# Kernel tuning notes

Measured on AMD Instinct MI355X. Metric: run time of the kernel, lower is better.

The kernel has to match this reference:

```python
import jax, jax.numpy as jnp
import numpy as np

BATCH = 32
N_LEVELS = (16384, 4096, 1024, 256)   # nodes at each mesh resolution
M_LEVELS = (4096, 1024, 256, 64)      # nodes after each Pool (downsample)
DEG = 6                               # directed edges per node
POOL_K = 3                            # nnz per row of downsample matrix
FILTERS = (3, 32, 32, 32, 64)         # channel chain of the 4 ChebConvs
K_CHEB = 6                            # Chebyshev polynomial order


def setup_inputs() -> dict:
    key = jax.random.key(0)
    ks = iter(jax.random.split(key, 64))
    inp = {"x": jax.random.normal(next(ks), (BATCH, N_LEVELS[0], FILTERS[0]), jnp.float32)}
    for i, N in enumerate(N_LEVELS):
        er = jnp.repeat(jnp.arange(N), DEG)
        off = jax.random.randint(next(ks), (N * DEG,), 1, N)
        inp[f"er{i}"] = er
        inp[f"ec{i}"] = (er + off) % N  # guaranteed no self loops
    for i, (M, N) in enumerate(zip(M_LEVELS, N_LEVELS)):
        inp[f"pr{i}"] = jnp.repeat(jnp.arange(M), POOL_K)
        inp[f"pc{i}"] = jax.random.randint(next(ks), (M * POOL_K,), 0, N)
        inp[f"pv{i}"] = jax.random.uniform(next(ks), (M * POOL_K,), jnp.float32)
    for i in range(4):
        fin, fout = FILTERS[i], FILTERS[i + 1]
        scale = 1.0 / np.sqrt(fin * K_CHEB)
        inp[f"W{i}"] = jax.random.normal(next(ks), (K_CHEB, fin, fout), jnp.float32) * scale
        inp[f"b{i}"] = jnp.zeros((fout,), jnp.float32)
    inp["enc_W"] = jax.random.normal(next(ks), (M_LEVELS[-1] * FILTERS[-1], 128), jnp.float32) * 0.1
    inp["enc_b"] = jnp.zeros((128,), jnp.float32)
    inp["cls_W"] = jax.random.normal(next(ks), (128, 10), jnp.float32) * 0.1
    inp["cls_b"] = jnp.zeros((10,), jnp.float32)
    return inp


def _cheb_conv(x, er, ec, W, b):
    # x: [B,N,Fin]; W: [K,Fin,Fout].
    # PyG ChebConv with lambda_max=2: L_hat = L - I = -D^{-1/2} A D^{-1/2}.
    N = x.shape[1]
    deg = jnp.zeros((N,), x.dtype).at[er].add(1.0)
    dinv = jnp.where(deg > 0, 1.0 / jnp.sqrt(jnp.maximum(deg, 1.0)), 0.0)
    norm = -(dinv[er] * dinv[ec])  # [E]

    def L(t):  # sparse matvec: gather neighbor feats, weight, scatter-add
        return jnp.zeros_like(t).at[:, er].add(t[:, ec] * norm[None, :, None])

    Tx0 = x
    out = jnp.einsum("bnf,fg->bng", Tx0, W[0])
    Tx1 = L(x)
    out = out + jnp.einsum("bnf,fg->bng", Tx1, W[1])
    for k in range(2, W.shape[0]):
        Tx2 = 2.0 * L(Tx1) - Tx0
        out = out + jnp.einsum("bnf,fg->bng", Tx2, W[k])
        Tx0, Tx1 = Tx1, Tx2
    return out + b


def _pool(x, pr, pc, pv, m):
    # sparse downsample matrix [m,N]: index_select cols * value, scatter_add rows
    B, _, F = x.shape
    return jnp.zeros((B, m, F), x.dtype).at[:, pr].add(x[:, pc] * pv[None, :, None])


def reference(x, er0, ec0, er1, ec1, er2, ec2, er3, ec3,
              pr0, pc0, pv0, pr1, pc1, pv1, pr2, pc2, pv2, pr3, pc3, pv3,
              W0, b0, W1, b1, W2, b2, W3, b3, enc_W, enc_b, cls_W, cls_b):
    ers, ecs = (er0, er1, er2, er3), (ec0, ec1, ec2, ec3)
    prs, pcs, pvs = (pr0, pr1, pr2, pr3), (pc0, pc1, pc2, pc3), (pv0, pv1, pv2, pv3)
    Ws, bs = (W0, W1, W2, W3), (b0, b1, b2, b3)
    for i in range(4):  # fixed n_layers loop (structurally distinct layers)
        x = jax.nn.relu(_cheb_conv(x, ers[i], ecs[i], Ws[i], bs[i]))
        x = _pool(x, prs[i], pcs[i], pvs[i], M_LEVELS[i])
    x = x.reshape(x.shape[0], -1)  # [B, 64*64]
    h = jax.nn.relu(x @ enc_W + enc_b)
    return h @ cls_W + cls_b
```

## Files before the change

kernel.cpp:

```cpp
#include <hip/hip_runtime.h>
#include <cstddef>
#include <cstdint>

#define BATCH 32


__device__ __forceinline__ void fma4(float4& a, float s, const float4& w) {
  a.x += s * w.x; a.y += s * w.y; a.z += s * w.z; a.w += s * w.w;
}
__device__ __forceinline__ float4 relu4(const float4& a) {
  return make_float4(fmaxf(a.x, 0.f), fmaxf(a.y, 0.f), fmaxf(a.z, 0.f), fmaxf(a.w, 0.f));
}

__global__ void __launch_bounds__(256) transpose_x(
    const float* __restrict__ x, float* __restrict__ xt)
{
  int t = blockIdx.x * 256 + threadIdx.x;
  int n = t / 96;
  int r = t % 96;
  int b = r / 3;
  int f = r - b * 3;
  xt[t] = x[((size_t)b * 16384 + n) * 3 + f];
}

template<int N, int R4>
__global__ void __launch_bounds__(256) cheb_step_nm(
    const float4* __restrict__ Tin, const float4* __restrict__ Tpp,
    const int* __restrict__ ec, float4* __restrict__ Tout,
    float coef, float beta)
{
  int idx = blockIdx.x * 256 + threadIdx.x;
  int n = idx / R4;
  int r = idx % R4;
  const int* e = ec + n * 6;
  float4 s = make_float4(0.f, 0.f, 0.f, 0.f);
#pragma unroll
  for (int d = 0; d < 6; ++d) {
    float4 v = Tin[(size_t)e[d] * R4 + r];
    s.x += v.x; s.y += v.y; s.z += v.z; s.w += v.w;
  }
  float4 p = Tpp[idx];
  float4 o;
  o.x = coef * s.x + beta * p.x;
  o.y = coef * s.y + beta * p.y;
  o.z = coef * s.z + beta * p.z;
  o.w = coef * s.w + beta * p.w;
  Tout[idx] = o;
}

template<int N, int F, int THREADS, int MINW>
__global__ void __launch_bounds__(THREADS, MINW) cheb_recur_reg(
    const float* __restrict__ X,
    const int* __restrict__ ec,
    float* __restrict__ T)
{
  constexpr int FS = 2;
  constexpr int NPT = N / THREADS;
  __shared__ float cur[N * FS];
  const float cI = -1.0f / 6.0f;
  const float cS = -1.0f / 3.0f;
  const int b = blockIdx.x & 31;
  const int fbase = (blockIdx.x >> 5) * FS;
  constexpr size_t SL = (size_t)N * 32 * F;
  float prevv[NPT][FS];
#pragma unroll
  for (int i = 0; i < NPT; ++i) {
    int n = threadIdx.x + i * THREADS;
    float2 v = *(const float2*)(X + ((size_t)n * 32 + b) * F + fbase);
    cur[n * FS + 0] = v.x;
    cur[n * FS + 1] = v.y;
  }
  __syncthreads();
#pragma unroll 1
  for (int k = 1; k <= 5; ++k) {
    float newv[NPT][FS];
    float* Tk = T + (size_t)(k - 1) * SL;
#pragma unroll
    for (int i = 0; i < NPT; ++i) {
      int n = threadIdx.x + i * THREADS;
      const int* e = ec + n * 6;
      float s0 = 0.f, s1 = 0.f;
#pragma unroll
      for (int d = 0; d < 6; ++d) {
        int c = e[d];
        s0 += cur[c * FS + 0];
        s1 += cur[c * FS + 1];
      }
      float v0, v1;
      if (k == 1) { v0 = cI * s0; v1 = cI * s1; }
      else        { v0 = cS * s0 - prevv[i][0]; v1 = cS * s1 - prevv[i][1]; }
      newv[i][0] = v0; newv[i][1] = v1;
      *(float2*)(Tk + ((size_t)n * 32 + b) * F + fbase) = make_float2(v0, v1);
    }
    __syncthreads();
#pragma unroll
    for (int i = 0; i < NPT; ++i) {
      int n = threadIdx.x + i * THREADS;
      prevv[i][0] = cur[n * FS + 0];
      prevv[i][1] = cur[n * FS + 1];
      cur[n * FS + 0] = newv[i][0];
      cur[n * FS + 1] = newv[i][1];
    }
    __syncthreads();
  }
}

template<int N, int M, int FOUT, bool OUT_BM>
__global__ void __launch_bounds__(256) pool_conv_f3(
    const float* __restrict__ X, const float* __restrict__ T,
    const float* __restrict__ W, const float* __restrict__ bias,
    const int* __restrict__ pc, const float* __restrict__ pv,
    float* __restrict__ out)
{
  constexpr int F4 = FOUT / 4;
  constexpr size_t SL = (size_t)N * BATCH * 3;
  __shared__ float Ws[6 * 3 * FOUT];
  for (int i = threadIdx.x; i < 6 * 3 * FOUT; i += 256) Ws[i] = W[i];
  __syncthreads();
  const float4* Ws4 = (const float4*)Ws;
  int t = blockIdx.x * 256 + threadIdx.x;
  int fo4 = t % F4;
  int b   = (t / F4) % BATCH;
  int m   = t / (F4 * BATCH);
  int c0 = pc[m * 3 + 0], c1 = pc[m * 3 + 1], c2 = pc[m * 3 + 2];
  float v0 = pv[m * 3 + 0], v1 = pv[m * 3 + 1], v2 = pv[m * 3 + 2];
  float4 bi = ((const float4*)bias)[fo4];
  float4 a0 = bi, a1 = bi, a2 = bi;
#pragma unroll
  for (int k = 0; k < 6; ++k) {
    const float* base = (k == 0) ? X : (T + (size_t)(k - 1) * SL);
    const float* r0 = base + ((size_t)c0 * BATCH + b) * 3;
    const float* r1 = base + ((size_t)c1 * BATCH + b) * 3;
    const float* r2 = base + ((size_t)c2 * BATCH + b) * 3;
#pragma unroll
    for (int f = 0; f < 3; ++f) {
      float4 w = Ws4[(k * 3 + f) * F4 + fo4];
      fma4(a0, r0[f], w);
      fma4(a1, r1[f], w);
      fma4(a2, r2[f], w);
    }
  }
  a0 = relu4(a0); a1 = relu4(a1); a2 = relu4(a2);
  float4 acc;
  acc.x = v0*a0.x + v1*a1.x + v2*a2.x;
  acc.y = v0*a0.y + v1*a1.y + v2*a2.y;
  acc.z = v0*a0.z + v1*a1.z + v2*a2.z;
  acc.w = v0*a0.w + v1*a1.w + v2*a2.w;
  size_t oi = OUT_BM ? (((size_t)b * M + m) * F4 + fo4) : (((size_t)m * BATCH + b) * F4 + fo4);
  ((float4*)out)[oi] = acc;
}

template<int N, int M, int FOUT, bool OUT_BM>
__global__ void __launch_bounds__(256) pool_conv_v32(
    const float* __restrict__ X, const float* __restrict__ T,
    const float* __restrict__ W, const float* __restrict__ bias,
    const int* __restrict__ pc, const float* __restrict__ pv,
    float* __restrict__ out)
{
  constexpr int FIN = 32;
  constexpr int F4 = FOUT / 4;
  constexpr size_t SL4 = (size_t)N * BATCH * FIN / 4;
  __shared__ float Ws[6 * FIN * FOUT];
  for (int i = threadIdx.x; i < 6 * FIN * FOUT; i += 256) Ws[i] = W[i];
  __syncthreads();
  const float4* Ws4 = (const float4*)Ws;
  const float4* X4p = (const float4*)X;
  const float4* T4s = (const float4*)T;
  int t = blockIdx.x * 256 + threadIdx.x;
  int fo4 = t % F4;
  int b   = (t / F4) % BATCH;
  int m   = t / (F4 * BATCH);
  int c0 = pc[m * 3 + 0], c1 = pc[m * 3 + 1], c2 = pc[m * 3 + 2];
  float v0 = pv[m * 3 + 0], v1 = pv[m * 3 + 1], v2 = pv[m * 3 + 2];
  float4 bi = ((const float4*)bias)[fo4];
  float4 a0 = bi, a1 = bi, a2 = bi;
#pragma unroll 1
  for (int k = 0; k < 6; ++k) {
    const float4* base = (k == 0) ? X4p : (T4s + (size_t)(k - 1) * SL4);
    const float4* r0 = base + ((size_t)c0 * BATCH + b) * 8;
    const float4* r1 = base + ((size_t)c1 * BATCH + b) * 8;
    const float4* r2 = base + ((size_t)c2 * BATCH + b) * 8;
#pragma unroll
    for (int fi = 0; fi < 8; ++fi) {
      float4 t0 = r0[fi], t1 = r1[fi], t2 = r2[fi];
#pragma unroll
      for (int ff = 0; ff < 4; ++ff) {
        float4 w = Ws4[((k * 32) + fi * 4 + ff) * F4 + fo4];
        fma4(a0, ((const float*)&t0)[ff], w);
        fma4(a1, ((const float*)&t1)[ff], w);
        fma4(a2, ((const float*)&t2)[ff], w);
      }
    }
  }
  a0 = relu4(a0); a1 = relu4(a1); a2 = relu4(a2);
  float4 acc;
  acc.x = v0*a0.x + v1*a1.x + v2*a2.x;
  acc.y = v0*a0.y + v1*a1.y + v2*a2.y;
  acc.z = v0*a0.z + v1*a1.z + v2*a2.z;
  acc.w = v0*a0.w + v1*a1.w + v2*a2.w;
  size_t oi = OUT_BM ? (((size_t)b * M + m) * F4 + fo4) : (((size_t)m * BATCH + b) * F4 + fo4);
  ((float4*)out)[oi] = acc;
}

__global__ void __launch_bounds__(256) encoder_partial(
    const float* __restrict__ Xf, const float* __restrict__ encW,
    float* __restrict__ partial)
{
  int b  = blockIdx.x;
  int ks = blockIdx.y;
  int fo = threadIdx.x & 127;
  int half = threadIdx.x >> 7;
  const float* xr = Xf + b * 4096 + ks * 256 + half * 128;
  const float* w  = encW + (size_t)(ks * 256 + half * 128) * 128;
  float acc = 0.f;
#pragma unroll 8
  for (int i = 0; i < 128; ++i) acc += xr[i] * w[(size_t)i * 128 + fo];
  __shared__ float part[256];
  part[threadIdx.x] = acc;
  __syncthreads();
  if (half == 0) partial[(size_t)(b * 16 + ks) * 128 + fo] = part[fo] + part[128 + fo];
}

__global__ void __launch_bounds__(128) encoder_reduce_cls(
    const float* __restrict__ partial, const float* __restrict__ encB,
    const float* __restrict__ clsW, const float* __restrict__ clsB,
    float* __restrict__ out)
{
  int b = blockIdx.x;
  int fo = threadIdx.x;
  float acc = encB[fo];
#pragma unroll
  for (int ks = 0; ks < 16; ++ks) acc += partial[(size_t)(b * 16 + ks) * 128 + fo];
  __shared__ float Hs[128];
  Hs[fo] = fmaxf(acc, 0.f);
  __syncthreads();
  if (fo < 10) {
    float s = clsB[fo];
#pragma unroll 4
    for (int f = 0; f < 128; ++f) s += Hs[f] * clsW[f * 10 + fo];
    out[b * 10 + fo] = s;
  }
}

extern "C" void kernel_launch(void* const* d_in, const int* in_sizes, int n_in,
                              void* d_out, int out_size, void* d_ws, size_t ws_size,
                              hipStream_t stream)
{
  const float* x   = (const float*)d_in[0];
  const int* ec0 = (const int*)d_in[2];
  const int* ec1 = (const int*)d_in[4];
  const int* ec2 = (const int*)d_in[6];
  const int* ec3 = (const int*)d_in[8];
  const int* pc0 = (const int*)d_in[10]; const float* pv0 = (const float*)d_in[11];
  const int* pc1 = (const int*)d_in[13]; const float* pv1 = (const float*)d_in[14];
  const int* pc2 = (const int*)d_in[16]; const float* pv2 = (const float*)d_in[17];
  const int* pc3 = (const int*)d_in[19]; const float* pv3 = (const float*)d_in[20];
  const float* W0 = (const float*)d_in[21]; const float* b0 = (const float*)d_in[22];
  const float* W1 = (const float*)d_in[23]; const float* b1 = (const float*)d_in[24];
  const float* W2 = (const float*)d_in[25]; const float* b2 = (const float*)d_in[26];
  const float* W3 = (const float*)d_in[27]; const float* b3 = (const float*)d_in[28];
  const float* encW = (const float*)d_in[29]; const float* encB = (const float*)d_in[30];
  const float* clsW = (const float*)d_in[31]; const float* clsB = (const float*)d_in[32];
  float* out = (float*)d_out;

  float* ws = (float*)d_ws;
  float* Xt = ws;
  float* T  = Xt + 1572864;
  float* X1 = T  + 20971520;
  float* X2 = X1 + 4194304;
  float* X3 = X2 + 1048576;
  float* X4 = X3 + 262144;
  float* P  = X4 + 131072;

  const float cI = -1.0f / 6.0f;
  const float cS = -1.0f / 3.0f;
  dim3 blk(256);

  transpose_x<<<dim3(6144), blk, 0, stream>>>(x, Xt);

  {
    constexpr size_t S = (size_t)16384 * 96;
    const float4* Xt4 = (const float4*)Xt;
    cheb_step_nm<16384, 24><<<dim3(1536), blk, 0, stream>>>(
        Xt4, Xt4, ec0, (float4*)T, cI, 0.f);
    cheb_step_nm<16384, 24><<<dim3(1536), blk, 0, stream>>>(
        (const float4*)T, Xt4, ec0, (float4*)(T + S), cS, -1.f);
    cheb_step_nm<16384, 24><<<dim3(1536), blk, 0, stream>>>(
        (const float4*)(T + S), (const float4*)T, ec0, (float4*)(T + 2 * S), cS, -1.f);
    cheb_step_nm<16384, 24><<<dim3(1536), blk, 0, stream>>>(
        (const float4*)(T + 2 * S), (const float4*)(T + S), ec0, (float4*)(T + 3 * S), cS, -1.f);
    cheb_step_nm<16384, 24><<<dim3(1536), blk, 0, stream>>>(
        (const float4*)(T + 3 * S), (const float4*)(T + 2 * S), ec0, (float4*)(T + 4 * S), cS, -1.f);
    pool_conv_f3<16384, 4096, 32, false><<<dim3(4096), blk, 0, stream>>>(
        Xt, T, W0, b0, pc0, pv0, X1);
  }
  {
    cheb_recur_reg<4096, 32, 512, 4><<<dim3(512), dim3(512), 0, stream>>>(X1, ec1, T);
    pool_conv_v32<4096, 1024, 32, false><<<dim3(1024), blk, 0, stream>>>(
        X1, T, W1, b1, pc1, pv1, X2);
  }
  {
    cheb_recur_reg<1024, 32, 256, 4><<<dim3(512), blk, 0, stream>>>(X2, ec2, T);
    pool_conv_v32<1024, 256, 32, false><<<dim3(256), blk, 0, stream>>>(
        X2, T, W2, b2, pc2, pv2, X3);
  }
  {
    cheb_recur_reg<256, 32, 256, 4><<<dim3(512), blk, 0, stream>>>(X3, ec3, T);
    pool_conv_v32<256, 64, 64, true><<<dim3(128), blk, 0, stream>>>(
        X3, T, W3, b3, pc3, pv3, X4);
  }
  encoder_partial<<<dim3(32, 16), blk, 0, stream>>>(X4, encW, P);
  encoder_reduce_cls<<<dim3(32), dim3(128), 0, stream>>>(P, encB, clsW, clsB, out);
}
```

Before: 326.4 us.

## Fuse level-0 Chebyshev recurrence into one LDS-resident kernel per batch-feature

Replaces the five separate global-memory Chebyshev step launches at the finest level with a single kernel. Each block keeps one (batch, feature) slice of 16384 nodes in shared memory and iterates all five recurrence steps there. This removes repeated global gathers and launch overhead. In exchange, it launches only 96 large blocks and writes outputs with a stride of 96 floats, which can underuse the GPU and give uncoalesced stores.

After: 422.0 us. +29.3%, slower.

```diff
diff --git a/kernel.cpp b/kernel.cpp
--- a/kernel.cpp
+++ b/kernel.cpp
@@ -23,29 +23,50 @@
   xt[t] = x[((size_t)b * 16384 + n) * 3 + f];
 }
 
-template<int N, int R4>
-__global__ void __launch_bounds__(256) cheb_step_nm(
-    const float4* __restrict__ Tin, const float4* __restrict__ Tpp,
-    const int* __restrict__ ec, float4* __restrict__ Tout,
-    float coef, float beta)
-{
-  int idx = blockIdx.x * 256 + threadIdx.x;
-  int n = idx / R4;
-  int r = idx % R4;
-  const int* e = ec + n * 6;
-  float4 s = make_float4(0.f, 0.f, 0.f, 0.f);
-#pragma unroll
-  for (int d = 0; d < 6; ++d) {
-    float4 v = Tin[(size_t)e[d] * R4 + r];
-    s.x += v.x; s.y += v.y; s.z += v.z; s.w += v.w;
-  }
-  float4 p = Tpp[idx];
-  float4 o;
-  o.x = coef * s.x + beta * p.x;
-  o.y = coef * s.y + beta * p.y;
-  o.z = coef * s.z + beta * p.z;
-  o.w = coef * s.w + beta * p.w;
-  Tout[idx] = o;
+template<int N, int THREADS, int MINW>
+__global__ void __launch_bounds__(THREADS, MINW) cheb_recur_f3(
+    const float* __restrict__ X,
+    const int* __restrict__ ec,
+    float* __restrict__ T)
+{
+  constexpr int NPT = N / THREADS;
+  __shared__ float cur[N];
+  const float cI = -1.0f / 6.0f;
+  const float cS = -1.0f / 3.0f;
+  const int b = blockIdx.x & 31;
+  const int f = blockIdx.x >> 5;
+  constexpr size_t SL = (size_t)N * 32 * 3;
+  float prevv[NPT];
+#pragma unroll
+  for (int i = 0; i < NPT; ++i) {
+    int n = threadIdx.x + i * THREADS;
+    cur[n] = X[((size_t)n * 32 + b) * 3 + f];
+  }
+  __syncthreads();
+#pragma unroll 1
+  for (int k = 1; k <= 5; ++k) {
+    float newv[NPT];
+    float* Tk = T + (size_t)(k - 1) * SL;
+#pragma unroll
+    for (int i = 0; i < NPT; ++i) {
+      int n = threadIdx.x + i * THREADS;
+      const int* e = ec + n * 6;
+      float s = 0.f;
+#pragma unroll
+      for (int d = 0; d < 6; ++d) s += cur[e[d]];
+      float v = (k == 1) ? (cI * s) : (cS * s - prevv[i]);
+      newv[i] = v;
+      Tk[((size_t)n * 32 + b) * 3 + f] = v;
+    }
+    __syncthreads();
+#pragma unroll
+    for (int i = 0; i < NPT; ++i) {
+      int n = threadIdx.x + i * THREADS;
+      prevv[i] = cur[n];
+      cur[n] = newv[i];
+    }
+    __syncthreads();
+  }
 }
 
 template<int N, int F, int THREADS, int MINW>
@@ -272,25 +293,12 @@
   float* X4 = X3 + 262144;
   float* P  = X4 + 131072;
 
-  const float cI = -1.0f / 6.0f;
-  const float cS = -1.0f / 3.0f;
   dim3 blk(256);
 
   transpose_x<<<dim3(6144), blk, 0, stream>>>(x, Xt);
 
   {
-    constexpr size_t S = (size_t)16384 * 96;
-    const float4* Xt4 = (const float4*)Xt;
-    cheb_step_nm<16384, 24><<<dim3(1536), blk, 0, stream>>>(
-        Xt4, Xt4, ec0, (float4*)T, cI, 0.f);
-    cheb_step_nm<16384, 24><<<dim3(1536), blk, 0, stream>>>(
-        (const float4*)T, Xt4, ec0, (float4*)(T + S), cS, -1.f);
-    cheb_step_nm<16384, 24><<<dim3(1536), blk, 0, stream>>>(
-        (const float4*)(T + S), (const float4*)T, ec0, (float4*)(T + 2 * S), cS, -1.f);
-    cheb_step_nm<16384, 24><<<dim3(1536), blk, 0, stream>>>(
-        (const float4*)(T + 2 * S), (const float4*)(T + S), ec0, (float4*)(T + 3 * S), cS, -1.f);
-    cheb_step_nm<16384, 24><<<dim3(1536), blk, 0, stream>>>(
-        (const float4*)(T + 3 * S), (const float4*)(T + 2 * S), ec0, (float4*)(T + 4 * S), cS, -1.f);
+    cheb_recur_f3<16384, 1024, 2><<<dim3(96), dim3(1024), 0, stream>>>(Xt, ec0, T);
     pool_conv_f3<16384, 4096, 32, false><<<dim3(4096), blk, 0, stream>>>(
         Xt, T, W0, b0, pc0, pv0, X1);
   }
```

## Store Chebyshev basis intermediates in fp16 with padded half4 layout

Applied to the files above, without the earlier changes.

All Chebyshev recurrence outputs T_k are now written as fp16, and the level-0 input is transposed into a padded 4-wide half layout (3 channels plus a zero). The recurrence and pool-conv kernels convert to fp32 for arithmetic. This roughly halves the bytes written and gathered for the large T buffers, which dominate memory traffic. In exchange it adds rounding error to the basis terms, which accumulates across the recurrence, and spends some extra work on conversions and the padding lane.

Result: faster. 319.2 us (-2.2%).

```diff
diff --git a/kernel.cpp b/kernel.cpp
--- a/kernel.cpp
+++ b/kernel.cpp
@@ -1,10 +1,18 @@
 #include <hip/hip_runtime.h>
+#include <hip/hip_fp16.h>
 #include <cstddef>
 #include <cstdint>
 
 #define BATCH 32
 
 
+struct alignas(8) half4 { __half2 lo, hi; };
+
+__device__ __forceinline__ void h4f(const half4 h, float f[4]) {
+  float2 a = __half22float2(h.lo);
+  float2 c = __half22float2(h.hi);
+  f[0] = a.x; f[1] = a.y; f[2] = c.x; f[3] = c.y;
+}
 __device__ __forceinline__ void fma4(float4& a, float s, const float4& w) {
   a.x += s * w.x; a.y += s * w.y; a.z += s * w.z; a.w += s * w.w;
 }
@@ -12,47 +20,96 @@
   return make_float4(fmaxf(a.x, 0.f), fmaxf(a.y, 0.f), fmaxf(a.z, 0.f), fmaxf(a.w, 0.f));
 }
 
-__global__ void __launch_bounds__(256) transpose_x(
-    const float* __restrict__ x, float* __restrict__ xt)
+__global__ void __launch_bounds__(256) transpose_h(
+    const float* __restrict__ x, half4* __restrict__ xh)
 {
   int t = blockIdx.x * 256 + threadIdx.x;
-  int n = t / 96;
-  int r = t % 96;
-  int b = r / 3;
-  int f = r - b * 3;
-  xt[t] = x[((size_t)b * 16384 + n) * 3 + f];
-}
-
-template<int N, int R4>
-__global__ void __launch_bounds__(256) cheb_step_nm(
-    const float4* __restrict__ Tin, const float4* __restrict__ Tpp,
-    const int* __restrict__ ec, float4* __restrict__ Tout,
+  int n = t >> 5;
+  int b = t & 31;
+  const float* src = x + ((size_t)b * 16384 + n) * 3;
+  half4 h;
+  h.lo = __floats2half2_rn(src[0], src[1]);
+  h.hi = __floats2half2_rn(src[2], 0.f);
+  xh[t] = h;
+}
+
+template<int N>
+__global__ void __launch_bounds__(256) cheb_step_h(
+    const half4* __restrict__ Tin, const half4* __restrict__ Tpp,
+    const int* __restrict__ ec, half4* __restrict__ Tout,
     float coef, float beta)
 {
   int idx = blockIdx.x * 256 + threadIdx.x;
-  int n = idx / R4;
-  int r = idx % R4;
+  int n = idx >> 5;
+  int b = idx & 31;
   const int* e = ec + n * 6;
-  float4 s = make_float4(0.f, 0.f, 0.f, 0.f);
+  float s0 = 0.f, s1 = 0.f, s2 = 0.f;
 #pragma unroll
   for (int d = 0; d < 6; ++d) {
-    float4 v = Tin[(size_t)e[d] * R4 + r];
-    s.x += v.x; s.y += v.y; s.z += v.z; s.w += v.w;
-  }
-  float4 p = Tpp[idx];
-  float4 o;
-  o.x = coef * s.x + beta * p.x;
-  o.y = coef * s.y + beta * p.y;
-  o.z = coef * s.z + beta * p.z;
-  o.w = coef * s.w + beta * p.w;
+    half4 v = Tin[(e[d] << 5) | b];
+    float2 a = __half22float2(v.lo);
+    float2 c = __half22float2(v.hi);
+    s0 += a.x; s1 += a.y; s2 += c.x;
+  }
+  half4 p = Tpp[idx];
+  float2 pa = __half22float2(p.lo);
+  float2 pc = __half22float2(p.hi);
+  half4 o;
+  o.lo = __floats2half2_rn(coef * s0 + beta * pa.x, coef * s1 + beta * pa.y);
+  o.hi = __floats2half2_rn(coef * s2 + beta * pc.x, 0.f);
   Tout[idx] = o;
 }
 
+template<int N, int M, int FOUT>
+__global__ void __launch_bounds__(256) pool_conv_f3_h(
+    const half4* __restrict__ Xh, const half4* __restrict__ T,
+    const float* __restrict__ W, const float* __restrict__ bias,
+    const int* __restrict__ pc, const float* __restrict__ pv,
+    float* __restrict__ out)
+{
+  constexpr int F4 = FOUT / 4;
+  constexpr size_t SL = (size_t)N * 32;
+  __shared__ float Ws[6 * 3 * FOUT];
+  for (int i = threadIdx.x; i < 6 * 3 * FOUT; i += 256) Ws[i] = W[i];
+  __syncthreads();
+  const float4* Ws4 = (const float4*)Ws;
+  int t = blockIdx.x * 256 + threadIdx.x;
+  int fo4 = t % F4;
+  int b   = (t / F4) % BATCH;
+  int m   = t / (F4 * BATCH);
+  int c0 = pc[m * 3 + 0], c1 = pc[m * 3 + 1], c2 = pc[m * 3 + 2];
+  float v0 = pv[m * 3 + 0], v1 = pv[m * 3 + 1], v2 = pv[m * 3 + 2];
+  float4 bi = ((const float4*)bias)[fo4];
+  float4 a0 = bi, a1 = bi, a2 = bi;
+#pragma unroll
+  for (int k = 0; k < 6; ++k) {
+    const half4* base = (k == 0) ? Xh : (T + (size_t)(k - 1) * SL);
+    float r0[4], r1[4], r2[4];
+    h4f(base[(c0 << 5) | b], r0);
+    h4f(base[(c1 << 5) | b], r1);
+    h4f(base[(c2 << 5) | b], r2);
+#pragma unroll
+    for (int f = 0; f < 3; ++f) {
+      float4 w = Ws4[(k * 3 + f) * F4 + fo4];
+      fma4(a0, r0[f], w);
+      fma4(a1, r1[f], w);
+      fma4(a2, r2[f], w);
+    }
+  }
+  a0 = relu4(a0); a1 = relu4(a1); a2 = relu4(a2);
+  float4 acc;
+  acc.x = v0*a0.x + v1*a1.x + v2*a2.x;
+  acc.y = v0*a0.y + v1*a1.y + v2*a2.y;
+  acc.z = v0*a0.z + v1*a1.z + v2*a2.z;
+  acc.w = v0*a0.w + v1*a1.w + v2*a2.w;
+  ((float4*)out)[((size_t)m * BATCH + b) * F4 + fo4] = acc;
+}
+
 template<int N, int F, int THREADS, int MINW>
-__global__ void __launch_bounds__(THREADS, MINW) cheb_recur_reg(
+__global__ void __launch_bounds__(THREADS, MINW) cheb_recur_h(
     const float* __restrict__ X,
     const int* __restrict__ ec,
-    float* __restrict__ T)
+    __half* __restrict__ Th)
 {
   constexpr int FS = 2;
   constexpr int NPT = N / THREADS;
@@ -61,7 +118,7 @@
   const float cS = -1.0f / 3.0f;
   const int b = blockIdx.x & 31;
   const int fbase = (blockIdx.x >> 5) * FS;
-  constexpr size_t SL = (size_t)N * 32 * F;
+  constexpr size_t SLH = (size_t)N * 32 * F;
   float prevv[NPT][FS];
 #pragma unroll
   for (int i = 0; i < NPT; ++i) {
@@ -74,7 +131,7 @@
 #pragma unroll 1
   for (int k = 1; k <= 5; ++k) {
     float newv[NPT][FS];
-    float* Tk = T + (size_t)(k - 1) * SL;
+    __half2* Tk2 = (__half2*)(Th + (size_t)(k - 1) * SLH);
 #pragma unroll
     for (int i = 0; i < NPT; ++i) {
       int n = threadIdx.x + i * THREADS;
@@ -90,7 +147,7 @@
       if (k == 1) { v0 = cI * s0; v1 = cI * s1; }
       else        { v0 = cS * s0 - prevv[i][0]; v1 = cS * s1 - prevv[i][1]; }
       newv[i][0] = v0; newv[i][1] = v1;
-      *(float2*)(Tk + ((size_t)n * 32 + b) * F + fbase) = make_float2(v0, v1);
+      Tk2[(((size_t)n * 32 + b) * F + fbase) >> 1] = __floats2half2_rn(v0, v1);
     }
     __syncthreads();
 #pragma unroll
@@ -106,18 +163,20 @@
 }
 
 template<int N, int M, int FOUT, bool OUT_BM>
-__global__ void __launch_bounds__(256) pool_conv_f3(
-    const float* __restrict__ X, const float* __restrict__ T,
+__global__ void __launch_bounds__(256) pool_conv_v32_h(
+    const float* __restrict__ X, const __half* __restrict__ Th,
     const float* __restrict__ W, const float* __restrict__ bias,
     const int* __restrict__ pc, const float* __restrict__ pv,
     float* __restrict__ out)
 {
+  constexpr int FIN = 32;
   constexpr int F4 = FOUT / 4;
-  constexpr size_t SL = (size_t)N * BATCH * 3;
-  __shared__ float Ws[6 * 3 * FOUT];
-  for (int i = threadIdx.x; i < 6 * 3 * FOUT; i += 256) Ws[i] = W[i];
+  constexpr size_t SLH = (size_t)N * 32 * FIN;
+  __shared__ float Ws[6 * FIN * FOUT];
+  for (int i = threadIdx.x; i < 6 * FIN * FOUT; i += 256) Ws[i] = W[i];
   __syncthreads();
   const float4* Ws4 = (const float4*)Ws;
+  const float4* X4p = (const float4*)X;
   int t = blockIdx.x * 256 + threadIdx.x;
   int fo4 = t % F4;
   int b   = (t / F4) % BATCH;
@@ -126,69 +185,38 @@
   float v0 = pv[m * 3 + 0], v1 = pv[m * 3 + 1], v2 = pv[m * 3 + 2];
   float4 bi = ((const float4*)bias)[fo4];
   float4 a0 = bi, a1 = bi, a2 = bi;
-#pragma unroll
-  for (int k = 0; k < 6; ++k) {
-    const float* base = (k == 0) ? X : (T + (size_t)(k - 1) * SL);
-    const float* r0 = base + ((size_t)c0 * BATCH + b) * 3;
-    const float* r1 = base + ((size_t)c1 * BATCH + b) * 3;
-    const float* r2 = base + ((size_t)c2 * BATCH + b) * 3;
-#pragma unroll
-    for (int f = 0; f < 3; ++f) {
-      float4 w = Ws4[(k * 3 + f) * F4 + fo4];
-      fma4(a0, r0[f], w);
-      fma4(a1, r1[f], w);
-      fma4(a2, r2[f], w);
-    }
-  }
-  a0 = relu4(a0); a1 = relu4(a1); a2 = relu4(a2);
-  float4 acc;
-  acc.x = v0*a0.x + v1*a1.x + v2*a2.x;
-  acc.y = v0*a0.y + v1*a1.y + v2*a2.y;
-  acc.z = v0*a0.z + v1*a1.z + v2*a2.z;
-  acc.w = v0*a0.w + v1*a1.w + v2*a2.w;
-  size_t oi = OUT_BM ? (((size_t)b * M + m) * F4 + fo4) : (((size_t)m * BATCH + b) * F4 + fo4);
-  ((float4*)out)[oi] = acc;
-}
-
-template<int N, int M, int FOUT, bool OUT_BM>
-__global__ void __launch_bounds__(256) pool_conv_v32(
-    const float* __restrict__ X, const float* __restrict__ T,
-    const float* __restrict__ W, const float* __restrict__ bias,
-    const int* __restrict__ pc, const float* __restrict__ pv,
-    float* __restrict__ out)
-{
-  constexpr int FIN = 32;
-  constexpr int F4 = FOUT / 4;
-  constexpr size_t SL4 = (size_t)N * BATCH * FIN / 4;
-  __shared__ float Ws[6 * FIN * FOUT];
-  for (int i = threadIdx.x; i < 6 * FIN * FOUT; i += 256) Ws[i] = W[i];
-  __syncthreads();
-  const float4* Ws4 = (const float4*)Ws;
-  const float4* X4p = (const float4*)X;
-  const float4* T4s = (const float4*)T;
-  int t = blockIdx.x * 256 + threadIdx.x;
-  int fo4 = t % F4;
-  int b   = (t / F4) % BATCH;
-  int m   = t / (F4 * BATCH);
-  int c0 = pc[m * 3 + 0], c1 = pc[m * 3 + 1], c2 = pc[m * 3 + 2];
-  float v0 = pv[m * 3 + 0], v1 = pv[m * 3 + 1], v2 = pv[m * 3 + 2];
-  float4 bi = ((const float4*)bias)[fo4];
-  float4 a0 = bi, a1 = bi, a2 = bi;
-#pragma unroll 1
-  for (int k = 0; k < 6; ++k) {
-    const float4* base = (k == 0) ? X4p : (T4s + (size_t)(k - 1) * SL4);
-    const float4* r0 = base + ((size_t)c0 * BATCH + b) * 8;
-    const float4* r1 = base + ((size_t)c1 * BATCH + b) * 8;
-    const float4* r2 = base + ((size_t)c2 * BATCH + b) * 8;
+  {
+    const float4* r0 = X4p + ((size_t)c0 * BATCH + b) * 8;
+    const float4* r1 = X4p + ((size_t)c1 * BATCH + b) * 8;
+    const float4* r2 = X4p + ((size_t)c2 * BATCH + b) * 8;
 #pragma unroll
     for (int fi = 0; fi < 8; ++fi) {
       float4 t0 = r0[fi], t1 = r1[fi], t2 = r2[fi];
 #pragma unroll
       for (int ff = 0; ff < 4; ++ff) {
-        float4 w = Ws4[((k * 32) + fi * 4 + ff) * F4 + fo4];
+        float4 w = Ws4[(fi * 4 + ff) * F4 + fo4];
         fma4(a0, ((const float*)&t0)[ff], w);
         fma4(a1, ((const float*)&t1)[ff], w);
         fma4(a2, ((const float*)&t2)[ff], w);
+      }
+    }
+  }
+#pragma unroll 1
+  for (int k = 1; k < 6; ++k) {
+    const half4* base = (const half4*)(Th + (size_t)(k - 1) * SLH);
+    const half4* r0 = base + ((size_t)c0 * 32 + b) * 8;
+    const half4* r1 = base + ((size_t)c1 * 32 + b) * 8;
+    const half4* r2 = base + ((size_t)c2 * 32 + b) * 8;
+#pragma unroll
+    for (int q = 0; q < 8; ++q) {
+      float f0[4], f1[4], f2[4];
+      h4f(r0[q], f0); h4f(r1[q], f1); h4f(r2[q], f2);
+#pragma unroll
+      for (int ff = 0; ff < 4; ++ff) {
+        float4 w = Ws4[((k * 32) + q * 4 + ff) * F4 + fo4];
+        fma4(a0, f0[ff], w);
+        fma4(a1, f1[ff], w);
+        fma4(a2, f2[ff], w);
       }
     }
   }
@@ -264,9 +292,9 @@
   float* out = (float*)d_out;
 
   float* ws = (float*)d_ws;
-  float* Xt = ws;
-  float* T  = Xt + 1572864;
-  float* X1 = T  + 20971520;
+  half4*  Xh = (half4*)ws;
+  __half* Th = (__half*)(ws + 1048576);
+  float* X1 = ws + 1048576 + 10485760;
   float* X2 = X1 + 4194304;
   float* X3 = X2 + 1048576;
   float* X4 = X3 + 262144;
@@ -276,38 +304,33 @@
   const float cS = -1.0f / 3.0f;
   dim3 blk(256);
 
-  transpose_x<<<dim3(6144), blk, 0, stream>>>(x, Xt);
-
-  {
-    constexpr size_t S = (size_t)16384 * 96;
-    const float4* Xt4 = (const float4*)Xt;
-    cheb_step_nm<16384, 24><<<dim3(1536), blk, 0, stream>>>(
-        Xt4, Xt4, ec0, (float4*)T, cI, 0.f);
-    cheb_step_nm<16384, 24><<<dim3(1536), blk, 0, stream>>>(
-        (const float4*)T, Xt4, ec0, (float4*)(T + S), cS, -1.f);
-    cheb_step_nm<16384, 24><<<dim3(1536), blk, 0, stream>>>(
-        (const float4*)(T + S), (const float4*)T, ec0, (float4*)(T + 2 * S), cS, -1.f);
-    cheb_step_nm<16384, 24><<<dim3(1536), blk, 0, stream>>>(
-        (const float4*)(T + 2 * S), (const float4*)(T + S), ec0, (float4*)(T + 3 * S), cS, -1.f);
-    cheb_step_nm<16384, 24><<<dim3(1536), blk, 0, stream>>>(
-        (const float4*)(T + 3 * S), (const float4*)(T + 2 * S), ec0, (float4*)(T + 4 * S), cS, -1.f);
-    pool_conv_f3<16384, 4096, 32, false><<<dim3(4096), blk, 0, stream>>>(
-        Xt, T, W0, b0, pc0, pv0, X1);
-  }
-  {
-    cheb_recur_reg<4096, 32, 512, 4><<<dim3(512), dim3(512), 0, stream>>>(X1, ec1, T);
-    pool_conv_v32<4096, 1024, 32, false><<<dim3(1024), blk, 0, stream>>>(
-        X1, T, W1, b1, pc1, pv1, X2);
-  }
-  {
-    cheb_recur_reg<1024, 32, 256, 4><<<dim3(512), blk, 0, stream>>>(X2, ec2, T);
-    pool_conv_v32<1024, 256, 32, false><<<dim3(256), blk, 0, stream>>>(
-        X2, T, W2, b2, pc2, pv2, X3);
-  }
-  {
-    cheb_recur_reg<256, 32, 256, 4><<<dim3(512), blk, 0, stream>>>(X3, ec3, T);
-    pool_conv_v32<256, 64, 64, true><<<dim3(128), blk, 0, stream>>>(
-        X3, T, W3, b3, pc3, pv3, X4);
+  transpose_h<<<dim3(2048), blk, 0, stream>>>(x, Xh);
+
+  {
+    constexpr size_t S = (size_t)16384 * 32;
+    half4* T4 = (half4*)Th;
+    cheb_step_h<16384><<<dim3(2048), blk, 0, stream>>>(Xh,       Xh,       ec0, T4,        cI,  0.f);
+    cheb_step_h<16384><<<dim3(2048), blk, 0, stream>>>(T4,       Xh,       ec0, T4 + S,    cS, -1.f);
+    cheb_step_h<16384><<<dim3(2048), blk, 0, stream>>>(T4 + S,   T4,       ec0, T4 + 2*S,  cS, -1.f);
+    cheb_step_h<16384><<<dim3(2048), blk, 0, stream>>>(T4 + 2*S, T4 + S,   ec0, T4 + 3*S,  cS, -1.f);
+    cheb_step_h<16384><<<dim3(2048), blk, 0, stream>>>(T4 + 3*S, T4 + 2*S, ec0, T4 + 4*S,  cS, -1.f);
+    pool_conv_f3_h<16384, 4096, 32><<<dim3(4096), blk, 0, stream>>>(
+        Xh, (const half4*)Th, W0, b0, pc0, pv0, X1);
+  }
+  {
+    cheb_recur_h<4096, 32, 512, 4><<<dim3(512), dim3(512), 0, stream>>>(X1, ec1, Th);
+    pool_conv_v32_h<4096, 1024, 32, false><<<dim3(1024), blk, 0, stream>>>(
+        X1, Th, W1, b1, pc1, pv1, X2);
+  }
+  {
+    cheb_recur_h<1024, 32, 256, 4><<<dim3(512), blk, 0, stream>>>(X2, ec2, Th);
+    pool_conv_v32_h<1024, 256, 32, false><<<dim3(256), blk, 0, stream>>>(
+        X2, Th, W2, b2, pc2, pv2, X3);
+  }
+  {
+    cheb_recur_h<256, 32, 256, 4><<<dim3(512), blk, 0, stream>>>(X3, ec3, Th);
+    pool_conv_v32_h<256, 64, 64, true><<<dim3(128), blk, 0, stream>>>(
+        X3, Th, W3, b3, pc3, pv3, X4);
   }
   encoder_partial<<<dim3(32, 16), blk, 0, stream>>>(X4, encW, P);
   encoder_reduce_cls<<<dim3(32), dim3(128), 0, stream>>>(P, encB, clsW, clsB, out);
```
